# Kernel tuning notes

Hardware: AMD Instinct MI355X
Metric: run time of the kernel (lower is better)

## Reference

```python
import jax, jax.numpy as jnp
import numpy as np

B, S, F, E, A = 8192, 200, 128, 64, 64
H1, H2, H3 = 128, 64, 32
EPS = 1e-5


def setup_inputs() -> dict:
    key = jax.random.key(0)
    ks = jax.random.split(key, 24)
    w = lambda k, shape: jax.random.normal(k, shape, dtype=jnp.float32) * 0.05
    inp = {
        'candidate_features': jax.random.normal(ks[0], (B, F), dtype=jnp.float32),
        'history_features': jax.random.normal(ks[1], (B, S, F), dtype=jnp.float32),
        'history_length': jax.random.randint(ks[2], (B,), 1, S + 1, dtype=jnp.int32),
        # item embedding linear
        'Wi': w(ks[3], (F, E)), 'bi': jnp.zeros((E,), jnp.float32),
        # additive attention
        'Wq': w(ks[4], (E, A)), 'Wk': w(ks[5], (E, A)), 'Wv': w(ks[6], (A,)),
        # MLP layer 1 (3E -> H1) + BN
        'W1': w(ks[7], (3 * E, H1)), 'b1': jnp.zeros((H1,), jnp.float32),
        'g1': jnp.ones((H1,), jnp.float32), 'be1': jnp.zeros((H1,), jnp.float32),
        'm1': w(ks[8], (H1,)), 'v1': jax.random.uniform(ks[9], (H1,), jnp.float32, 0.5, 1.5),
        # MLP layer 2 (H1 -> H2) + BN
        'W2': w(ks[10], (H1, H2)), 'b2': jnp.zeros((H2,), jnp.float32),
        'g2': jnp.ones((H2,), jnp.float32), 'be2': jnp.zeros((H2,), jnp.float32),
        'm2': w(ks[11], (H2,)), 'v2': jax.random.uniform(ks[12], (H2,), jnp.float32, 0.5, 1.5),
        # MLP layer 3 (H2 -> H3) + BN
        'W3': w(ks[13], (H2, H3)), 'b3': jnp.zeros((H3,), jnp.float32),
        'g3': jnp.ones((H3,), jnp.float32), 'be3': jnp.zeros((H3,), jnp.float32),
        'm3': w(ks[14], (H3,)), 'v3': jax.random.uniform(ks[15], (H3,), jnp.float32, 0.5, 1.5),
        # output layer
        'Wo': w(ks[16], (H3, 1)), 'bo': jnp.zeros((1,), jnp.float32),
    }
    return inp


def _bn(x, g, be, m, v):
    # BatchNorm1d in eval mode (running stats)
    return (x - m) * jax.lax.rsqrt(v + EPS) * g + be


def reference(candidate_features, history_features, history_length,
              Wi, bi, Wq, Wk, Wv,
              W1, b1, g1, be1, m1, v1,
              W2, b2, g2, be2, m2, v2,
              W3, b3, g3, be3, m3, v3,
              Wo, bo):
    # item embedding
    cand = candidate_features @ Wi + bi          # [B, E]
    hist = history_features @ Wi + bi            # [B, S, E]

    # additive (Bahdanau) attention
    qh = cand @ Wq                               # [B, A]
    kh = hist @ Wk                               # [B, S, A]
    hidden = jax.nn.relu(qh[:, None, :] + kh)    # [B, S, A]
    scores = hidden @ Wv                         # [B, S]

    seq = jnp.arange(hist.shape[1])
    mask = seq[None, :] < history_length[:, None]  # [B, S] bool
    scores = jnp.where(mask, scores, -1e9)
    attn = jax.nn.softmax(scores, axis=1)        # [B, S]
    interest = jnp.einsum('bs,bse->be', attn, hist)  # [B, E]

    # mean pooling over valid history
    lens = history_length[:, None].astype(hist.dtype)
    avg = jnp.sum(hist * mask[:, :, None], axis=1) / lens  # [B, E]

    x = jnp.concatenate([interest, cand, avg], axis=1)     # [B, 3E]
    x = jax.nn.relu(_bn(x @ W1 + b1, g1, be1, m1, v1))
    x = jax.nn.relu(_bn(x @ W2 + b2, g2, be2, m2, v2))
    x = jax.nn.relu(_bn(x @ W3 + b3, g3, be3, m3, v3))
    logits = x @ Wo + bo                                   # [B, 1]
    return jax.nn.sigmoid(logits)[:, 0]                    # [B]
```

## Files before the change

kernel.cpp:

```cpp
#include <hip/hip_runtime.h>
#include <math.h>

#define Bn 8192
#define Sn 200
#define Fn 128
#define En 64
#define An 64
#define H1n 128
#define H2n 64
#define H3n 32
#define EPSn 1e-5f

typedef __attribute__((ext_vector_type(8))) short bf16x8;
typedef __attribute__((ext_vector_type(4))) float f32x4;

__device__ __forceinline__ uint pack_bf2(float a, float b) {
    uint ua = __float_as_uint(a), ub = __float_as_uint(b);
    ua += 0x7fffu + ((ua >> 16) & 1u);
    ub += 0x7fffu + ((ub >> 16) & 1u);
    return (ua >> 16) | (ub & 0xffff0000u);
}
__device__ __forceinline__ ushort bf16_1(float a) {
    uint u = __float_as_uint(a);
    u += 0x7fffu + ((u >> 16) & 1u);
    return (ushort)(u >> 16);
}

__global__ void k_mm(const float* __restrict__ Wi, const float* __restrict__ bi,
                     const float* __restrict__ Wk, const float* __restrict__ Wq,
                     ushort* __restrict__ wikp, ushort* __restrict__ wiqp,
                     float* __restrict__ bq) {
    int idx = blockIdx.x * 256 + threadIdx.x;
    int j = idx & 7, l = (idx >> 3) & 63, t = idx >> 9;
    int k = t & 3, ct = t >> 2;
    int row = k * 32 + 8 * (l >> 4) + j;
    int col = ct * 16 + (l & 15);
    float sk = 0.f, sq = 0.f;
    for (int e = 0; e < En; ++e) {
        float w = Wi[row * En + e];
        sk = fmaf(w, Wk[e * An + col], sk);
        sq = fmaf(w, Wq[e * An + col], sq);
    }
    wikp[idx] = bf16_1(sk);
    wiqp[idx] = bf16_1(sq);
    if (idx < An) {
        float s = 0.f;
        for (int e = 0; e < En; ++e) s = fmaf(bi[e], Wq[e * An + idx] + Wk[e * An + idx], s);
        bq[idx] = s;
    }
}

__global__ void k_pack(const float* __restrict__ src, ushort* __restrict__ dst,
                       int N, int nk, int total) {
    int p = blockIdx.x * 256 + threadIdx.x;
    if (p >= total) return;
    int j = p & 7, l = (p >> 3) & 63, t = p >> 9;
    int k = t % nk, ct = t / nk;
    int row = k * 32 + 8 * (l >> 4) + j;
    int col = ct * 16 + (l & 15);
    dst[p] = bf16_1(src[row * N + col]);
}

__global__ void k_bn(const float* __restrict__ b, const float* __restrict__ g,
                     const float* __restrict__ be, const float* __restrict__ m,
                     const float* __restrict__ v, float* __restrict__ al,
                     float* __restrict__ bt, int n) {
    int i = blockIdx.x * 256 + threadIdx.x;
    if (i < n) {
        float a = g[i] * rsqrtf(v[i] + EPSn);
        al[i] = a;
        bt[i] = (b[i] - m[i]) * a + be[i];
    }
}

__global__ __launch_bounds__(256, 4) void k_embed(
    const float* __restrict__ cand, const ushort* __restrict__ wip,
    const ushort* __restrict__ wiqp, const float* __restrict__ bi,
    const float* __restrict__ bq, ushort* __restrict__ ce, float* __restrict__ qhb) {
    const int tid = threadIdx.x, wv = tid >> 6, lane = tid & 63;
    const int rb = blockIdx.x * 64;
    __shared__ uint c_l[64 * 64];
    for (int i = tid; i < 2048; i += 256) {
        int row = i >> 5, f4 = i & 31;
        float4 v = ((const float4*)(cand + (size_t)(rb + row) * Fn))[f4];
        uint2 pw; pw.x = pack_bf2(v.x, v.y); pw.y = pack_bf2(v.z, v.w);
        int dw = (2 * f4) ^ ((row & 7) << 2);
        *(uint2*)&c_l[row * 64 + dw] = pw;
    }
    __syncthreads();
    const int r = wv * 16 + (lane & 15);
    bf16x8 afr[4];
    #pragma unroll
    for (int k = 0; k < 4; ++k)
        afr[k] = *(const bf16x8*)&c_l[r * 64 + ((k * 16 + 4 * (lane >> 4)) ^ ((r & 7) << 2))];
    #pragma unroll
    for (int ct = 0; ct < 4; ++ct) {
        f32x4 acc = {0.f, 0.f, 0.f, 0.f};
        #pragma unroll
        for (int k = 0; k < 4; ++k) {
            bf16x8 bfr = *(const bf16x8*)&wip[((ct * 4 + k) * 64 + lane) * 8];
            acc = __builtin_amdgcn_mfma_f32_16x16x32_bf16(afr[k], bfr, acc, 0, 0, 0);
        }
        int col = ct * 16 + (lane & 15);
        float bic = bi[col];
        #pragma unroll
        for (int i = 0; i < 4; ++i) {
            int rg = rb + wv * 16 + (lane >> 4) * 4 + i;
            ce[(size_t)rg * 64 + col] = bf16_1(acc[i] + bic);
        }
    }
    #pragma unroll
    for (int ct = 0; ct < 4; ++ct) {
        f32x4 acc = {0.f, 0.f, 0.f, 0.f};
        #pragma unroll
        for (int k = 0; k < 4; ++k) {
            bf16x8 bfr = *(const bf16x8*)&wiqp[((ct * 4 + k) * 64 + lane) * 8];
            acc = __builtin_amdgcn_mfma_f32_16x16x32_bf16(afr[k], bfr, acc, 0, 0, 0);
        }
        int col = ct * 16 + (lane & 15);
        float bqc = bq[col];
        #pragma unroll
        for (int i = 0; i < 4; ++i) {
            int rg = rb + wv * 16 + (lane >> 4) * 4 + i;
            qhb[(size_t)rg * 64 + col] = acc[i] + bqc;
        }
    }
}

__global__ __launch_bounds__(256, 4) void k_main(
    const float* __restrict__ hist, const int* __restrict__ hlen,
    const float* __restrict__ qhb, const float* __restrict__ Wv,
    const ushort* __restrict__ wikp, ushort* __restrict__ ifav) {
    const int b = blockIdx.x;
    const int tid = threadIdx.x, wv = tid >> 6, lane = tid & 63;
    __shared__ uint wik_l[4096];
    __shared__ alignas(16) uint h_u[64 * 64];
    __shared__ alignas(16) float w_sc[64];
    __shared__ float s_d[4];
    __shared__ float s_acc[4][Fn], s_sum[4][Fn];

    {
        const uint4* wp = (const uint4*)wikp;
        for (int q = tid; q < 1024; q += 256) {
            uint4 v = wp[q];
            int l = q & 63;
            int dw = (q * 4) ^ (((l >> 3) & 3) << 2);
            *(uint4*)&wik_l[dw] = v;
        }
    }

    const int len = hlen[b];
    const float* hb = hist + (size_t)b * Sn * Fn;

    float qhb_l[4], wv_l[4];
    #pragma unroll
    for (int ct = 0; ct < 4; ++ct) {
        qhb_l[ct] = qhb[(size_t)b * 64 + ct * 16 + (lane & 15)];
        wv_l[ct] = Wv[ct * 16 + (lane & 15)];
    }

    float m = -3.0e38f, d = 0.f;
    float accx = 0.f, accy = 0.f, sumx = 0.f, sumy = 0.f;
    const int nch = (len + 63) >> 6;

    for (int c = 0; c < nch; ++c) {
        const int sc0 = c * 64;
        for (int i = tid; i < 2048; i += 256) {
            int sl = i >> 5, f4 = i & 31;
            int sg = sc0 + sl;
            float4 v = (sg < len) ? ((const float4*)(hb + (size_t)sg * Fn))[f4]
                                  : make_float4(0.f, 0.f, 0.f, 0.f);
            uint2 pw;
            pw.x = pack_bf2(v.x, v.y);
            pw.y = pack_bf2(v.z, v.w);
            int dw = (2 * f4) ^ ((sl & 7) << 2);
            *(uint2*)&h_u[sl * 64 + dw] = pw;
        }
        __syncthreads();
        {
            const int r = wv * 16 + (lane & 15);
            bf16x8 afr[4];
            #pragma unroll
            for (int k = 0; k < 4; ++k)
                afr[k] = *(const bf16x8*)&h_u[r * 64 + ((k * 16 + 4 * (lane >> 4)) ^ ((r & 7) << 2))];
            float contrib[4] = {0.f, 0.f, 0.f, 0.f};
            #pragma unroll
            for (int ct = 0; ct < 4; ++ct) {
                f32x4 acc = {0.f, 0.f, 0.f, 0.f};
                #pragma unroll
                for (int k = 0; k < 4; ++k) {
                    bf16x8 bfr = *(const bf16x8*)&wik_l[(((ct * 4 + k) * 64 + lane) * 4) ^ (((lane >> 3) & 3) << 2)];
                    acc = __builtin_amdgcn_mfma_f32_16x16x32_bf16(afr[k], bfr, acc, 0, 0, 0);
                }
                float qv = qhb_l[ct], wvv = wv_l[ct];
                #pragma unroll
                for (int rr = 0; rr < 4; ++rr)
                    contrib[rr] += fmaxf(acc[rr] + qv, 0.f) * wvv;
            }
            #pragma unroll
            for (int o = 1; o < 16; o <<= 1) {
                #pragma unroll
                for (int rr = 0; rr < 4; ++rr)
                    contrib[rr] += __shfl_xor(contrib[rr], o, 64);
            }
            if ((lane & 15) == 0) {
                #pragma unroll
                for (int rr = 0; rr < 4; ++rr) {
                    int jr = wv * 16 + (lane >> 4) * 4 + rr;
                    w_sc[jr] = (sc0 + jr < len) ? contrib[rr] : -1e30f;
                }
            }
        }
        __syncthreads();
        {
            const f32x4* wsp = (const f32x4*)w_sc;
            float mloc = -3.0e38f;
            #pragma unroll
            for (int q = 0; q < 16; ++q) {
                f32x4 s = wsp[q];
                mloc = fmaxf(mloc, fmaxf(fmaxf(s[0], s[1]), fmaxf(s[2], s[3])));
            }
            float mn = fmaxf(m, mloc);
            float cc = __expf(m - mn);
            m = mn;
            d *= cc; accx *= cc; accy *= cc;
            #pragma unroll
            for (int j = 0; j < 16; ++j) {
                int sl = 4 * j + wv;
                float wgt = __expf(w_sc[sl] - mn);
                d += wgt;
                uint hv = h_u[sl * 64 + (lane ^ ((sl & 7) << 2))];
                float hx = __uint_as_float(hv << 16);
                float hy = __uint_as_float(hv & 0xffff0000u);
                accx = fmaf(wgt, hx, accx);
                accy = fmaf(wgt, hy, accy);
                sumx += hx; sumy += hy;
            }
        }
        __syncthreads();
    }

    if (lane == 0) s_d[wv] = d;
    s_acc[wv][2 * lane + 0] = accx;
    s_acc[wv][2 * lane + 1] = accy;
    s_sum[wv][2 * lane + 0] = sumx;
    s_sum[wv][2 * lane + 1] = sumy;
    __syncthreads();
    if (tid < Fn) {
        float D = s_d[0] + s_d[1] + s_d[2] + s_d[3];
        float A = s_acc[0][tid] + s_acc[1][tid] + s_acc[2][tid] + s_acc[3][tid];
        float S = s_sum[0][tid] + s_sum[1][tid] + s_sum[2][tid] + s_sum[3][tid];
        ifav[(size_t)b * 256 + tid] = bf16_1(A / D);
        ifav[(size_t)b * 256 + 128 + tid] = bf16_1(S / (float)len);
    }
}

__global__ __launch_bounds__(256, 2) void k_mlp(
    const ushort* __restrict__ ifav, const ushort* __restrict__ ce,
    const float* __restrict__ bi, const ushort* __restrict__ wip,
    const ushort* __restrict__ w1p, const ushort* __restrict__ w2p,
    const ushort* __restrict__ w3p,
    const float* __restrict__ al1, const float* __restrict__ bt1,
    const float* __restrict__ al2, const float* __restrict__ bt2,
    const float* __restrict__ al3, const float* __restrict__ bt3,
    const float* __restrict__ Wo, const float* __restrict__ bo,
    float* __restrict__ out) {
    const int tid = threadIdx.x, wv = tid >> 6, lane = tid & 63;
    const int rb = blockIdx.x * 64;
    __shared__ uint x_l[64 * 96];
    __shared__ uint h1_l[64 * 64];
    __shared__ uint h2_l[64 * 32];
    __shared__ uint h3_l[64 * 16];
    ushort* x_s = (ushort*)x_l;
    ushort* h1_s = (ushort*)h1_l;
    ushort* h2_s = (ushort*)h2_l;
    ushort* h3_s = (ushort*)h3_l;

    const int rloc = wv * 16 + (lane & 15);

    #pragma unroll
    for (int half = 0; half < 2; ++half) {
        bf16x8 afr[4];
        #pragma unroll
        for (int k = 0; k < 4; ++k)
            afr[k] = *(const bf16x8*)&ifav[(size_t)(rb + rloc) * 256 + half * 128 + k * 32 + 8 * (lane >> 4)];
        #pragma unroll
        for (int ct = 0; ct < 4; ++ct) {
            f32x4 acc = {0.f, 0.f, 0.f, 0.f};
            #pragma unroll
            for (int k = 0; k < 4; ++k) {
                bf16x8 bfr = *(const bf16x8*)&wip[((ct * 4 + k) * 64 + lane) * 8];
                acc = __builtin_amdgcn_mfma_f32_16x16x32_bf16(afr[k], bfr, acc, 0, 0, 0);
            }
            int col = ct * 16 + (lane & 15);
            float bic = bi[col];
            int xcol = half * 128 + col;
            #pragma unroll
            for (int i = 0; i < 4; ++i) {
                int row = wv * 16 + (lane >> 4) * 4 + i;
                int dd = (xcol >> 1) ^ ((row & 7) << 2);
                x_s[(row * 96 + dd) * 2 + (xcol & 1)] = bf16_1(acc[i] + bic);
            }
        }
    }
    {
        int rl = wv * 16 + (lane >> 2);
        int colb = (lane & 3) * 16;
        #pragma unroll
        for (int u = 0; u < 2; ++u) {
            uint4 v = *(const uint4*)&ce[(size_t)(rb + rl) * 64 + colb + u * 8];
            int db = (32 + (lane & 3) * 8 + u * 4) ^ ((rl & 7) << 2);
            *(uint4*)&x_l[rl * 96 + db] = v;
        }
    }
    {
        bf16x8 xa[6];
        #pragma unroll
        for (int k = 0; k < 6; ++k)
            xa[k] = *(const bf16x8*)&x_l[rloc * 96 + ((k * 16 + 4 * (lane >> 4)) ^ ((rloc & 7) << 2))];
        #pragma unroll
        for (int ct = 0; ct < 8; ++ct) {
            f32x4 acc = {0.f, 0.f, 0.f, 0.f};
            #pragma unroll
            for (int k = 0; k < 6; ++k) {
                bf16x8 bfr = *(const bf16x8*)&w1p[((ct * 6 + k) * 64 + lane) * 8];
                acc = __builtin_amdgcn_mfma_f32_16x16x32_bf16(xa[k], bfr, acc, 0, 0, 0);
            }
            int col = ct * 16 + (lane & 15);
            float a = al1[col], bt = bt1[col];
            #pragma unroll
            for (int i = 0; i < 4; ++i) {
                int row = wv * 16 + (lane >> 4) * 4 + i;
                float hv = fmaxf(fmaf(acc[i], a, bt), 0.f);
                int dd = (col >> 1) ^ ((row & 7) << 2);
                h1_s[(row * 64 + dd) * 2 + (col & 1)] = bf16_1(hv);
            }
        }
    }
    {
        bf16x8 xa[4];
        #pragma unroll
        for (int k = 0; k < 4; ++k)
            xa[k] = *(const bf16x8*)&h1_l[rloc * 64 + ((k * 16 + 4 * (lane >> 4)) ^ ((rloc & 7) << 2))];
        #pragma unroll
        for (int ct = 0; ct < 4; ++ct) {
            f32x4 acc = {0.f, 0.f, 0.f, 0.f};
            #pragma unroll
            for (int k = 0; k < 4; ++k) {
                bf16x8 bfr = *(const bf16x8*)&w2p[((ct * 4 + k) * 64 + lane) * 8];
                acc = __builtin_amdgcn_mfma_f32_16x16x32_bf16(xa[k], bfr, acc, 0, 0, 0);
            }
            int col = ct * 16 + (lane & 15);
            float a = al2[col], bt = bt2[col];
            #pragma unroll
            for (int i = 0; i < 4; ++i) {
                int row = wv * 16 + (lane >> 4) * 4 + i;
                float hv = fmaxf(fmaf(acc[i], a, bt), 0.f);
                int dd = (col >> 1) ^ ((row & 7) << 2);
                h2_s[(row * 32 + dd) * 2 + (col & 1)] = bf16_1(hv);
            }
        }
    }
    {
        bf16x8 xa[2];
        #pragma unroll
        for (int k = 0; k < 2; ++k)
            xa[k] = *(const bf16x8*)&h2_l[rloc * 32 + ((k * 16 + 4 * (lane >> 4)) ^ ((rloc & 7) << 2))];
        #pragma unroll
        for (int ct = 0; ct < 2; ++ct) {
            f32x4 acc = {0.f, 0.f, 0.f, 0.f};
            #pragma unroll
            for (int k = 0; k < 2; ++k) {
                bf16x8 bfr = *(const bf16x8*)&w3p[((ct * 2 + k) * 64 + lane) * 8];
                acc = __builtin_amdgcn_mfma_f32_16x16x32_bf16(xa[k], bfr, acc, 0, 0, 0);
            }
            int col = ct * 16 + (lane & 15);
            float a = al3[col], bt = bt3[col];
            #pragma unroll
            for (int i = 0; i < 4; ++i) {
                int row = wv * 16 + (lane >> 4) * 4 + i;
                float hv = fmaxf(fmaf(acc[i], a, bt), 0.f);
                int dd = (col >> 1) ^ ((row & 3) << 2);
                h3_s[(row * 16 + dd) * 2 + (col & 1)] = bf16_1(hv);
            }
        }
    }
    if (lane < 16) {
        int row = wv * 16 + lane;
        float acc = bo[0];
        #pragma unroll
        for (int dd = 0; dd < 16; ++dd) {
            uint hv = h3_l[row * 16 + (dd ^ ((row & 3) << 2))];
            float h0 = __uint_as_float(hv << 16);
            float h1 = __uint_as_float(hv & 0xffff0000u);
            acc = fmaf(h0, Wo[2 * dd], fmaf(h1, Wo[2 * dd + 1], acc));
        }
        out[rb + row] = 1.f / (1.f + __expf(-acc));
    }
}

extern "C" void kernel_launch(void* const* d_in, const int* in_sizes, int n_in,
                              void* d_out, int out_size, void* d_ws, size_t ws_size,
                              hipStream_t stream) {
    const float* cand = (const float*)d_in[0];
    const float* hist = (const float*)d_in[1];
    const int*   hlen = (const int*)d_in[2];
    const float* Wi = (const float*)d_in[3];
    const float* bi = (const float*)d_in[4];
    const float* Wq = (const float*)d_in[5];
    const float* Wk = (const float*)d_in[6];
    const float* Wv = (const float*)d_in[7];
    const float* W1 = (const float*)d_in[8];
    const float* b1 = (const float*)d_in[9];
    const float* g1 = (const float*)d_in[10];
    const float* be1 = (const float*)d_in[11];
    const float* m1 = (const float*)d_in[12];
    const float* v1 = (const float*)d_in[13];
    const float* W2 = (const float*)d_in[14];
    const float* b2 = (const float*)d_in[15];
    const float* g2 = (const float*)d_in[16];
    const float* be2 = (const float*)d_in[17];
    const float* m2 = (const float*)d_in[18];
    const float* v2 = (const float*)d_in[19];
    const float* W3 = (const float*)d_in[20];
    const float* b3 = (const float*)d_in[21];
    const float* g3 = (const float*)d_in[22];
    const float* be3 = (const float*)d_in[23];
    const float* m3 = (const float*)d_in[24];
    const float* v3 = (const float*)d_in[25];
    const float* Wo = (const float*)d_in[26];
    const float* bo = (const float*)d_in[27];
    float* out = (float*)d_out;

    char* ws = (char*)d_ws;
    ushort* wikp = (ushort*)(ws + 0);
    ushort* wiqp = (ushort*)(ws + 16384);
    ushort* wip  = (ushort*)(ws + 32768);
    ushort* w1p  = (ushort*)(ws + 49152);
    ushort* w2p  = (ushort*)(ws + 98304);
    ushort* w3p  = (ushort*)(ws + 114688);
    float*  bq   = (float*)(ws + 118784);
    float*  al1  = (float*)(ws + 119040);
    float*  bt1  = (float*)(ws + 119552);
    float*  al2  = (float*)(ws + 120064);
    float*  bt2  = (float*)(ws + 120320);
    float*  al3  = (float*)(ws + 120576);
    float*  bt3  = (float*)(ws + 120704);
    float*  qhb  = (float*)(ws + 131072);
    ushort* ce   = (ushort*)(ws + 131072 + 2097152);
    ushort* ifav = (ushort*)(ws + 131072 + 3145728);

    k_mm<<<32, 256, 0, stream>>>(Wi, bi, Wk, Wq, wikp, wiqp, bq);
    k_pack<<<32, 256, 0, stream>>>(Wi, wip, 64, 4, 8192);
    k_pack<<<96, 256, 0, stream>>>(W1, w1p, 128, 6, 24576);
    k_pack<<<32, 256, 0, stream>>>(W2, w2p, 64, 4, 8192);
    k_pack<<<8, 256, 0, stream>>>(W3, w3p, 32, 2, 2048);
    k_bn<<<1, 256, 0, stream>>>(b1, g1, be1, m1, v1, al1, bt1, H1n);
    k_bn<<<1, 256, 0, stream>>>(b2, g2, be2, m2, v2, al2, bt2, H2n);
    k_bn<<<1, 256, 0, stream>>>(b3, g3, be3, m3, v3, al3, bt3, H3n);
    k_embed<<<Bn / 64, 256, 0, stream>>>(cand, wip, wiqp, bi, bq, ce, qhb);
    k_main<<<Bn, 256, 0, stream>>>(hist, hlen, qhb, Wv, wikp, ifav);
    k_mlp<<<Bn / 64, 256, 0, stream>>>(ifav, ce, bi, wip, w1p, w2p, w3p,
                                       al1, bt1, al2, bt2, al3, bt3, Wo, bo, out);
}
```

Before: 189.2 us.

## Prefetch next history chunk into registers, double-buffer LDS, merge prep kernels

The main attention kernel now prefetches the next 64-row history chunk into registers while the current chunk is processed. It double-buffers the shared-memory tile so one barrier per chunk can be dropped, and it reuses the weight LDS region for the final reduction. Occupancy is lowered to 3 blocks per CU to make room for the extra registers and LDS. The eight small weight-packing and batch-norm prep launches are fused into one kernel to cut launch overhead.

```diff
diff --git a/kernel.cpp b/kernel.cpp
--- a/kernel.cpp
+++ b/kernel.cpp
@@ -14,6 +14,10 @@
 typedef __attribute__((ext_vector_type(8))) short bf16x8;
 typedef __attribute__((ext_vector_type(4))) float f32x4;
 
+#define BARR() do { asm volatile("s_waitcnt lgkmcnt(0)" ::: "memory"); \
+                    __builtin_amdgcn_s_barrier(); \
+                    asm volatile("" ::: "memory"); } while (0)
+
 __device__ __forceinline__ uint pack_bf2(float a, float b) {
     uint ua = __float_as_uint(a), ub = __float_as_uint(b);
     ua += 0x7fffu + ((ua >> 16) & 1u);
@@ -26,34 +30,9 @@
     return (ushort)(u >> 16);
 }
 
-__global__ void k_mm(const float* __restrict__ Wi, const float* __restrict__ bi,
-                     const float* __restrict__ Wk, const float* __restrict__ Wq,
-                     ushort* __restrict__ wikp, ushort* __restrict__ wiqp,
-                     float* __restrict__ bq) {
-    int idx = blockIdx.x * 256 + threadIdx.x;
-    int j = idx & 7, l = (idx >> 3) & 63, t = idx >> 9;
-    int k = t & 3, ct = t >> 2;
-    int row = k * 32 + 8 * (l >> 4) + j;
-    int col = ct * 16 + (l & 15);
-    float sk = 0.f, sq = 0.f;
-    for (int e = 0; e < En; ++e) {
-        float w = Wi[row * En + e];
-        sk = fmaf(w, Wk[e * An + col], sk);
-        sq = fmaf(w, Wq[e * An + col], sq);
-    }
-    wikp[idx] = bf16_1(sk);
-    wiqp[idx] = bf16_1(sq);
-    if (idx < An) {
-        float s = 0.f;
-        for (int e = 0; e < En; ++e) s = fmaf(bi[e], Wq[e * An + idx] + Wk[e * An + idx], s);
-        bq[idx] = s;
-    }
-}
-
-__global__ void k_pack(const float* __restrict__ src, ushort* __restrict__ dst,
-                       int N, int nk, int total) {
-    int p = blockIdx.x * 256 + threadIdx.x;
-    if (p >= total) return;
+__device__ __forceinline__ void pack_frag(const float* __restrict__ src,
+                                          ushort* __restrict__ dst,
+                                          int p, int N, int nk) {
     int j = p & 7, l = (p >> 3) & 63, t = p >> 9;
     int k = t % nk, ct = t / nk;
     int row = k * 32 + 8 * (l >> 4) + j;
@@ -61,15 +40,68 @@
     dst[p] = bf16_1(src[row * N + col]);
 }
 
-__global__ void k_bn(const float* __restrict__ b, const float* __restrict__ g,
-                     const float* __restrict__ be, const float* __restrict__ m,
-                     const float* __restrict__ v, float* __restrict__ al,
-                     float* __restrict__ bt, int n) {
-    int i = blockIdx.x * 256 + threadIdx.x;
-    if (i < n) {
-        float a = g[i] * rsqrtf(v[i] + EPSn);
-        al[i] = a;
-        bt[i] = (b[i] - m[i]) * a + be[i];
+__global__ void k_prep(
+    const float* __restrict__ Wi, const float* __restrict__ bi,
+    const float* __restrict__ Wk, const float* __restrict__ Wq,
+    const float* __restrict__ W1, const float* __restrict__ W2,
+    const float* __restrict__ W3,
+    const float* __restrict__ b1, const float* __restrict__ g1,
+    const float* __restrict__ be1, const float* __restrict__ m1,
+    const float* __restrict__ v1,
+    const float* __restrict__ b2, const float* __restrict__ g2,
+    const float* __restrict__ be2, const float* __restrict__ m2,
+    const float* __restrict__ v2,
+    const float* __restrict__ b3, const float* __restrict__ g3,
+    const float* __restrict__ be3, const float* __restrict__ m3,
+    const float* __restrict__ v3,
+    ushort* __restrict__ wikp, ushort* __restrict__ wiqp, float* __restrict__ bq,
+    ushort* __restrict__ wip, ushort* __restrict__ w1p,
+    ushort* __restrict__ w2p, ushort* __restrict__ w3p,
+    float* __restrict__ al1, float* __restrict__ bt1,
+    float* __restrict__ al2, float* __restrict__ bt2,
+    float* __restrict__ al3, float* __restrict__ bt3) {
+    const int blk = blockIdx.x, tid = threadIdx.x;
+    if (blk < 32) {
+        int idx = blk * 256 + tid;
+        int j = idx & 7, l = (idx >> 3) & 63, t = idx >> 9;
+        int k = t & 3, ct = t >> 2;
+        int row = k * 32 + 8 * (l >> 4) + j;
+        int col = ct * 16 + (l & 15);
+        float sk = 0.f, sq = 0.f;
+        for (int e = 0; e < En; ++e) {
+            float w = Wi[row * En + e];
+            sk = fmaf(w, Wk[e * An + col], sk);
+            sq = fmaf(w, Wq[e * An + col], sq);
+        }
+        wikp[idx] = bf16_1(sk);
+        wiqp[idx] = bf16_1(sq);
+        if (idx < An) {
+            float s = 0.f;
+            for (int e = 0; e < En; ++e)
+                s = fmaf(bi[e], Wq[e * An + idx] + Wk[e * An + idx], s);
+            bq[idx] = s;
+        }
+    } else if (blk < 64) {
+        pack_frag(Wi, wip, (blk - 32) * 256 + tid, 64, 4);
+    } else if (blk < 160) {
+        pack_frag(W1, w1p, (blk - 64) * 256 + tid, 128, 6);
+    } else if (blk < 192) {
+        pack_frag(W2, w2p, (blk - 160) * 256 + tid, 64, 4);
+    } else if (blk < 200) {
+        pack_frag(W3, w3p, (blk - 192) * 256 + tid, 32, 2);
+    } else {
+        if (tid < H1n) {
+            float a = g1[tid] * rsqrtf(v1[tid] + EPSn);
+            al1[tid] = a; bt1[tid] = (b1[tid] - m1[tid]) * a + be1[tid];
+        } else if (tid < H1n + H2n) {
+            int i = tid - H1n;
+            float a = g2[i] * rsqrtf(v2[i] + EPSn);
+            al2[i] = a; bt2[i] = (b2[i] - m2[i]) * a + be2[i];
+        } else if (tid < H1n + H2n + H3n) {
+            int i = tid - H1n - H2n;
+            float a = g3[i] * rsqrtf(v3[i] + EPSn);
+            al3[i] = a; bt3[i] = (b3[i] - m3[i]) * a + be3[i];
+        }
     }
 }
 
@@ -127,18 +159,27 @@
     }
 }
 
-__global__ __launch_bounds__(256, 4) void k_main(
+__global__ __launch_bounds__(256, 3) void k_main(
     const float* __restrict__ hist, const int* __restrict__ hlen,
     const float* __restrict__ qhb, const float* __restrict__ Wv,
     const ushort* __restrict__ wikp, ushort* __restrict__ ifav) {
     const int b = blockIdx.x;
     const int tid = threadIdx.x, wv = tid >> 6, lane = tid & 63;
     __shared__ uint wik_l[4096];
-    __shared__ alignas(16) uint h_u[64 * 64];
+    __shared__ alignas(16) uint h_u[2][64 * 64];
     __shared__ alignas(16) float w_sc[64];
-    __shared__ float s_d[4];
-    __shared__ float s_acc[4][Fn], s_sum[4][Fn];
-
+
+    const int len = hlen[b];
+    const float* hb = hist + (size_t)b * Sn * Fn;
+
+    float4 pv[8];
+    #pragma unroll
+    for (int q = 0; q < 8; ++q) {
+        int i = tid + q * 256;
+        int sl = i >> 5, f4 = i & 31;
+        pv[q] = (sl < len) ? ((const float4*)(hb + (size_t)sl * Fn))[f4]
+                           : make_float4(0.f, 0.f, 0.f, 0.f);
+    }
     {
         const uint4* wp = (const uint4*)wikp;
         for (int q = tid; q < 1024; q += 256) {
@@ -148,10 +189,6 @@
             *(uint4*)&wik_l[dw] = v;
         }
     }
-
-    const int len = hlen[b];
-    const float* hb = hist + (size_t)b * Sn * Fn;
-
     float qhb_l[4], wv_l[4];
     #pragma unroll
     for (int ct = 0; ct < 4; ++ct) {
@@ -162,27 +199,38 @@
     float m = -3.0e38f, d = 0.f;
     float accx = 0.f, accy = 0.f, sumx = 0.f, sumy = 0.f;
     const int nch = (len + 63) >> 6;
+    int buf = 0;
 
     for (int c = 0; c < nch; ++c) {
+        uint* hw = h_u[buf];
         const int sc0 = c * 64;
-        for (int i = tid; i < 2048; i += 256) {
+        #pragma unroll
+        for (int q = 0; q < 8; ++q) {
+            int i = tid + q * 256;
             int sl = i >> 5, f4 = i & 31;
-            int sg = sc0 + sl;
-            float4 v = (sg < len) ? ((const float4*)(hb + (size_t)sg * Fn))[f4]
-                                  : make_float4(0.f, 0.f, 0.f, 0.f);
             uint2 pw;
-            pw.x = pack_bf2(v.x, v.y);
-            pw.y = pack_bf2(v.z, v.w);
+            pw.x = pack_bf2(pv[q].x, pv[q].y);
+            pw.y = pack_bf2(pv[q].z, pv[q].w);
             int dw = (2 * f4) ^ ((sl & 7) << 2);
-            *(uint2*)&h_u[sl * 64 + dw] = pw;
-        }
-        __syncthreads();
+            *(uint2*)&hw[sl * 64 + dw] = pw;
+        }
+        if (c + 1 < nch) {
+            const int nb = sc0 + 64;
+            #pragma unroll
+            for (int q = 0; q < 8; ++q) {
+                int i = tid + q * 256;
+                int sl = nb + (i >> 5), f4 = i & 31;
+                pv[q] = (sl < len) ? ((const float4*)(hb + (size_t)sl * Fn))[f4]
+                                   : make_float4(0.f, 0.f, 0.f, 0.f);
+            }
+        }
+        BARR();
         {
             const int r = wv * 16 + (lane & 15);
             bf16x8 afr[4];
             #pragma unroll
             for (int k = 0; k < 4; ++k)
-                afr[k] = *(const bf16x8*)&h_u[r * 64 + ((k * 16 + 4 * (lane >> 4)) ^ ((r & 7) << 2))];
+                afr[k] = *(const bf16x8*)&hw[r * 64 + ((k * 16 + 4 * (lane >> 4)) ^ ((r & 7) << 2))];
             float contrib[4] = {0.f, 0.f, 0.f, 0.f};
             #pragma unroll
             for (int ct = 0; ct < 4; ++ct) {
@@ -211,7 +259,7 @@
                 }
             }
         }
-        __syncthreads();
+        BARR();
         {
             const f32x4* wsp = (const f32x4*)w_sc;
             float mloc = -3.0e38f;
@@ -229,7 +277,7 @@
                 int sl = 4 * j + wv;
                 float wgt = __expf(w_sc[sl] - mn);
                 d += wgt;
-                uint hv = h_u[sl * 64 + (lane ^ ((sl & 7) << 2))];
+                uint hv = hw[sl * 64 + (lane ^ ((sl & 7) << 2))];
                 float hx = __uint_as_float(hv << 16);
                 float hy = __uint_as_float(hv & 0xffff0000u);
                 accx = fmaf(wgt, hx, accx);
@@ -237,19 +285,20 @@
                 sumx += hx; sumy += hy;
             }
         }
-        __syncthreads();
-    }
-
-    if (lane == 0) s_d[wv] = d;
-    s_acc[wv][2 * lane + 0] = accx;
-    s_acc[wv][2 * lane + 1] = accy;
-    s_sum[wv][2 * lane + 0] = sumx;
-    s_sum[wv][2 * lane + 1] = sumy;
+        buf ^= 1;
+    }
+
+    float* mrg = (float*)wik_l;
+    if (lane == 0) mrg[wv] = d;
+    mrg[8 + wv * Fn + 2 * lane + 0] = accx;
+    mrg[8 + wv * Fn + 2 * lane + 1] = accy;
+    mrg[520 + wv * Fn + 2 * lane + 0] = sumx;
+    mrg[520 + wv * Fn + 2 * lane + 1] = sumy;
     __syncthreads();
     if (tid < Fn) {
-        float D = s_d[0] + s_d[1] + s_d[2] + s_d[3];
-        float A = s_acc[0][tid] + s_acc[1][tid] + s_acc[2][tid] + s_acc[3][tid];
-        float S = s_sum[0][tid] + s_sum[1][tid] + s_sum[2][tid] + s_sum[3][tid];
+        float D = mrg[0] + mrg[1] + mrg[2] + mrg[3];
+        float A = mrg[8 + tid] + mrg[8 + Fn + tid] + mrg[8 + 2 * Fn + tid] + mrg[8 + 3 * Fn + tid];
+        float S = mrg[520 + tid] + mrg[520 + Fn + tid] + mrg[520 + 2 * Fn + tid] + mrg[520 + 3 * Fn + tid];
         ifav[(size_t)b * 256 + tid] = bf16_1(A / D);
         ifav[(size_t)b * 256 + 128 + tid] = bf16_1(S / (float)len);
     }
@@ -450,14 +499,12 @@
     ushort* ce   = (ushort*)(ws + 131072 + 2097152);
     ushort* ifav = (ushort*)(ws + 131072 + 3145728);
 
-    k_mm<<<32, 256, 0, stream>>>(Wi, bi, Wk, Wq, wikp, wiqp, bq);
-    k_pack<<<32, 256, 0, stream>>>(Wi, wip, 64, 4, 8192);
-    k_pack<<<96, 256, 0, stream>>>(W1, w1p, 128, 6, 24576);
-    k_pack<<<32, 256, 0, stream>>>(W2, w2p, 64, 4, 8192);
-    k_pack<<<8, 256, 0, stream>>>(W3, w3p, 32, 2, 2048);
-    k_bn<<<1, 256, 0, stream>>>(b1, g1, be1, m1, v1, al1, bt1, H1n);
-    k_bn<<<1, 256, 0, stream>>>(b2, g2, be2, m2, v2, al2, bt2, H2n);
-    k_bn<<<1, 256, 0, stream>>>(b3, g3, be3, m3, v3, al3, bt3, H3n);
+    k_prep<<<201, 256, 0, stream>>>(Wi, bi, Wk, Wq, W1, W2, W3,
+                                    b1, g1, be1, m1, v1,
+                                    b2, g2, be2, m2, v2,
+                                    b3, g3, be3, m3, v3,
+                                    wikp, wiqp, bq, wip, w1p, w2p, w3p,
+                                    al1, bt1, al2, bt2, al3, bt3);
     k_embed<<<Bn / 64, 256, 0, stream>>>(cand, wip, wiqp, bi, bq, ce, qhb);
     k_main<<<Bn, 256, 0, stream>>>(hist, hlen, qhb, Wv, wikp, ifav);
     k_mlp<<<Bn / 64, 256, 0, stream>>>(ifav, ce, bi, wip, w1p, w2p, w3p,
```

New measurement: 199.0 us. 1.05x slower.
